# Optimization experiments

Measured on AMD Instinct MI355X. Metric: run time of the kernel, lower is better.

The kernel has to match this reference:

```python
import jax, jax.numpy as jnp
import numpy as np

D_MODEL = 1024
NUM_HEADS = 16
D_K = D_MODEL // NUM_HEADS
THETA = 10000.0
MAX_SEQ_LEN = 2048
BATCH = 2
SEQ = 2048


def setup_inputs() -> dict:
    key = jax.random.key(0)
    ks = jax.random.split(key, 5)
    std = np.sqrt(2.0 / (D_MODEL + D_MODEL)).astype(np.float32)
    x = jax.random.normal(ks[0], (BATCH, SEQ, D_MODEL), dtype=jnp.float32)
    Wq = jax.random.normal(ks[1], (D_MODEL, D_MODEL), dtype=jnp.float32) * std
    Wk = jax.random.normal(ks[2], (D_MODEL, D_MODEL), dtype=jnp.float32) * std
    Wv = jax.random.normal(ks[3], (D_MODEL, D_MODEL), dtype=jnp.float32) * std
    Wo = jax.random.normal(ks[4], (D_MODEL, D_MODEL), dtype=jnp.float32) * std
    token_positions = jnp.arange(SEQ, dtype=jnp.int32)
    return {"x": x, "token_positions": token_positions,
            "Wq": Wq, "Wk": Wk, "Wv": Wv, "Wo": Wo}


def _rope_tables(positions):
    # freqs: [d_k/2]; angles: [seq, d_k/2]
    freqs = 1.0 / (THETA ** (jnp.arange(0, D_K, 2, dtype=jnp.float32) / D_K))
    angles = positions.astype(jnp.float32)[:, None] * freqs[None, :]
    return jnp.cos(angles), jnp.sin(angles)


def _apply_rope(t, cos, sin):
    # t: [b, h, s, d_k]; cos/sin: [s, d_k/2]; interleaved pair rotation
    x1 = t[..., 0::2]
    x2 = t[..., 1::2]
    r1 = x1 * cos - x2 * sin
    r2 = x1 * sin + x2 * cos
    return jnp.stack([r1, r2], axis=-1).reshape(t.shape)


def reference(x, token_positions, Wq, Wk, Wv, Wo):
    b, s, _ = x.shape
    # projections: y = x W^T
    q = jnp.einsum('bsi,oi->bso', x, Wq)
    k = jnp.einsum('bsi,oi->bso', x, Wk)
    v = jnp.einsum('bsi,oi->bso', x, Wv)
    # split heads: [b, h, s, d]
    q = q.reshape(b, s, NUM_HEADS, D_K).transpose(0, 2, 1, 3)
    k = k.reshape(b, s, NUM_HEADS, D_K).transpose(0, 2, 1, 3)
    v = v.reshape(b, s, NUM_HEADS, D_K).transpose(0, 2, 1, 3)
    cos, sin = _rope_tables(token_positions)
    q = _apply_rope(q, cos, sin)
    k = _apply_rope(k, cos, sin)
    scale = jnp.asarray(D_K, jnp.float32) ** 0.5
    scores = jnp.einsum('bhqd,bhkd->bhqk', q, k) / scale
    causal = jnp.tril(jnp.ones((s, s), dtype=bool))
    scores = jnp.where(causal, scores, -jnp.inf)
    attn = jax.nn.softmax(scores.astype(jnp.float32), axis=-1).astype(scores.dtype)
    out = jnp.einsum('bhqk,bhkd->bhqd', attn, v)
    out = out.transpose(0, 2, 1, 3).reshape(b, s, D_MODEL)
    return jnp.einsum('bsi,oi->bso', out, Wo)
```

## Files before the change

### kernel.cpp

```cpp
#include <hip/hip_runtime.h>
#include <stdint.h>

#define D_MODEL 1024
#define NH      16
#define DKH     64
#define SEQLEN  2048
#define BATCH   2
#define KDIM    1024

typedef __attribute__((ext_vector_type(8))) short          short8;
typedef __attribute__((ext_vector_type(8))) unsigned short ushort8;
typedef __attribute__((ext_vector_type(4))) float          f32x4;

__device__ __forceinline__ unsigned short f2bf(float f) {
    union { float f; unsigned u; } v; v.f = f;
    unsigned u = v.u;
    unsigned r = (u + 0x7FFFu + ((u >> 16) & 1u)) >> 16;
    return (unsigned short)r;
}
__device__ __forceinline__ float bf2f(unsigned short h) {
    union { unsigned u; float f; } v; v.u = ((unsigned)h) << 16;
    return v.f;
}

__device__ __forceinline__ void gload_lds16(const unsigned short* g, unsigned short* l) {
    __builtin_amdgcn_global_load_lds(
        (__attribute__((address_space(1))) void*)(g),
        (__attribute__((address_space(3))) void*)(l), 16, 0, 0);
}

__global__ void cvt_all(const float* __restrict__ X,  const float* __restrict__ Wq,
                        const float* __restrict__ Wk, const float* __restrict__ Wv,
                        const float* __restrict__ Wo,
                        unsigned short* __restrict__ Xb,  unsigned short* __restrict__ Wqb,
                        unsigned short* __restrict__ Wkb, unsigned short* __restrict__ Wvb,
                        unsigned short* __restrict__ Wob) {
    const int z = blockIdx.y;
    const float* src; unsigned short* dst; int n;
    if (z == 0)      { src = X;  dst = Xb;  n = 4194304; }
    else if (z == 1) { src = Wq; dst = Wqb; n = 1048576; }
    else if (z == 2) { src = Wk; dst = Wkb; n = 1048576; }
    else if (z == 3) { src = Wv; dst = Wvb; n = 1048576; }
    else             { src = Wo; dst = Wob; n = 1048576; }
    int i = (blockIdx.x * 256 + threadIdx.x) * 8;
    if (i >= n) return;
    float4 a = *(const float4*)(src + i);
    float4 b = *(const float4*)(src + i + 4);
    ushort8 o;
    o[0] = f2bf(a.x); o[1] = f2bf(a.y); o[2] = f2bf(a.z); o[3] = f2bf(a.w);
    o[4] = f2bf(b.x); o[5] = f2bf(b.y); o[6] = f2bf(b.z); o[7] = f2bf(b.w);
    *(ushort8*)(dst + i) = o;
}

__device__ __forceinline__ void gemm_core_128(
    const unsigned short* __restrict__ A, const unsigned short* __restrict__ W,
    unsigned short* a_lds, unsigned short* b_lds,
    int m0, int n0, f32x4 acc[4][4])
{
    const int tid  = threadIdx.x;
    const int lane = tid & 63;
    const int w    = tid >> 6;
    const int quad = lane >> 4;
    const int l16  = lane & 15;
    const int wm   = w & 1, wn = w >> 1;

    const int srow = lane >> 2;
    const int scol = (lane & 3) * 8;

    #pragma unroll
    for (int mi = 0; mi < 4; mi++)
        #pragma unroll
        for (int ni = 0; ni < 4; ni++) {
            f32x4 z = {0.f, 0.f, 0.f, 0.f};
            acc[mi][ni] = z;
        }

    for (int kk = 0; kk < KDIM; kk += 32) {
        __syncthreads();
        #pragma unroll
        for (int i = 0; i < 2; ++i) {
            int c = 2 * w + i;
            gload_lds16(A + (size_t)(m0 + c * 16 + srow) * KDIM + kk + scol, &a_lds[c * 512]);
            gload_lds16(W + (size_t)(n0 + c * 16 + srow) * KDIM + kk + scol, &b_lds[c * 512]);
        }
        __syncthreads();

        short8 af[4], bf[4];
        #pragma unroll
        for (int i = 0; i < 4; i++) {
            af[i] = *(const short8*)&a_lds[(wm * 64 + i * 16 + l16) * 32 + quad * 8];
            bf[i] = *(const short8*)&b_lds[(wn * 64 + i * 16 + l16) * 32 + quad * 8];
        }
        #pragma unroll
        for (int mi = 0; mi < 4; mi++)
            #pragma unroll
            for (int ni = 0; ni < 4; ni++)
                acc[mi][ni] = __builtin_amdgcn_mfma_f32_16x16x32_bf16(af[mi], bf[ni], acc[mi][ni], 0, 0, 0);
    }
}

__global__ __launch_bounds__(256, 2)
void gemm_qkv(const unsigned short* __restrict__ X,
              const unsigned short* __restrict__ Wq,
              const unsigned short* __restrict__ Wk,
              const unsigned short* __restrict__ Wv,
              unsigned short* __restrict__ q_ws,
              unsigned short* __restrict__ k_ws,
              unsigned short* __restrict__ v_ws)
{
    __shared__ __align__(16) unsigned short a_lds[128 * 32];
    __shared__ __align__(16) unsigned short b_lds[128 * 32];

    const int z = blockIdx.z;
    const unsigned short* W = (z == 0) ? Wq : ((z == 1) ? Wk : Wv);
    const int m0 = blockIdx.x * 128, n0 = blockIdx.y * 128;

    f32x4 acc[4][4];
    gemm_core_128(X, W, a_lds, b_lds, m0, n0, acc);

    const int lane = threadIdx.x & 63;
    const int w    = threadIdx.x >> 6;
    const int quad = lane >> 4;
    const int l16  = lane & 15;
    const int wm   = w & 1, wn = w >> 1;

    #pragma unroll
    for (int mi = 0; mi < 4; mi++)
        #pragma unroll
        for (int ni = 0; ni < 4; ni++)
            #pragma unroll
            for (int r = 0; r < 4; r++) {
                int row = m0 + wm * 64 + mi * 16 + quad * 4 + r;
                int col = n0 + wn * 64 + ni * 16 + l16;
                int b = row >> 11, s = row & 2047;
                int h = col >> 6,  d = col & 63;
                int bh = b * NH + h;
                float val = acc[mi][ni][r];
                if (z == 2) {
                    v_ws[(size_t)bh * DKH * SEQLEN + (size_t)d * SEQLEN + s] = f2bf(val);
                } else {
                    unsigned short* dst = (z == 0) ? q_ws : k_ws;
                    dst[(size_t)bh * SEQLEN * DKH + (size_t)s * DKH + d] = f2bf(val);
                }
            }
}

__global__ void rope_kernel(const int* __restrict__ pos,
                            unsigned short* __restrict__ q_ws,
                            unsigned short* __restrict__ k_ws)
{
    int i = blockIdx.x * 256 + threadIdx.x;
    unsigned short* t = (i >> 19) ? k_ws : q_ws;
    int c   = i & 0x7FFFF;
    int bh  = c >> 14;
    int rem = c & 16383;
    int s   = rem >> 3;
    int ch  = rem & 7;
    size_t base = (size_t)bh * (SEQLEN * DKH) + (size_t)s * DKH + ch * 8;

    ushort8 v = *(ushort8*)(t + base);
    float p = (float)pos[s];
    ushort8 o;
    #pragma unroll
    for (int u = 0; u < 4; u++) {
        int j = ch * 4 + u;
        float freq = expf(-((float)(2 * j) * (1.0f / 64.0f)) * 9.210340371976184f);
        float ang = p * freq;
        float sn, cn;
        sincosf(ang, &sn, &cn);
        float x1 = bf2f(v[2 * u]);
        float x2 = bf2f(v[2 * u + 1]);
        o[2 * u]     = f2bf(x1 * cn - x2 * sn);
        o[2 * u + 1] = f2bf(x1 * sn + x2 * cn);
    }
    *(ushort8*)(t + base) = o;
}

__global__ __launch_bounds__(256, 2)
void attn_kernel(const unsigned short* __restrict__ q_ws,
                 const unsigned short* __restrict__ k_ws,
                 const unsigned short* __restrict__ v_ws,
                 unsigned short* __restrict__ ao)
{
    __shared__ __align__(16) unsigned short k_lds[128 * 72];
    __shared__ __align__(16) unsigned short v_lds[64 * 136];
    __shared__ __align__(16) unsigned short p_lds[4 * 16 * 136];

    const int bh  = blockIdx.x;
    const int p   = blockIdx.y;
    const int tid = threadIdx.x, lane = tid & 63, w = tid >> 6;
    const int quad = lane >> 4, l16 = lane & 15;

    const size_t kqbase = (size_t)bh * SEQLEN * DKH;
    const size_t vbase  = (size_t)bh * DKH * SEQLEN;
    const int b = bh >> 4, h = bh & 15;

    const int krow = tid >> 3, kcol = (tid & 7) * 8;
    const int vrow = tid >> 4, vcol = (tid & 15) * 8;

    #pragma unroll
    for (int phase = 0; phase < 2; ++phase) {
        const int qt  = (phase == 0) ? (31 - p) : p;
        const int q0  = qt * 64;
        const int qw0 = q0 + w * 16;
        const int nt  = (qt + 2) >> 1;

        short8 aq[2];
        #pragma unroll
        for (int kc = 0; kc < 2; kc++)
            aq[kc] = *(const short8*)(q_ws + kqbase + (size_t)(qw0 + l16) * DKH + kc * 32 + quad * 8);

        f32x4 o_acc[4];
        #pragma unroll
        for (int df = 0; df < 4; df++) { f32x4 z = {0.f,0.f,0.f,0.f}; o_acc[df] = z; }
        float l_i[4] = {0.f, 0.f, 0.f, 0.f};

        ushort8 kreg[4], vreg[4];
        #pragma unroll
        for (int rr = 0; rr < 4; ++rr) {
            kreg[rr] = *(const ushort8*)(k_ws + kqbase + (size_t)(krow + rr * 32) * DKH + kcol);
            vreg[rr] = *(const ushort8*)(v_ws + vbase + (size_t)(vrow + rr * 16) * SEQLEN + vcol);
        }

        for (int t = 0; t < nt; ++t) {
            const int s0 = t * 128;
            __syncthreads();
            #pragma unroll
            for (int rr = 0; rr < 4; ++rr) {
                *(ushort8*)&k_lds[(krow + rr * 32) * 72 + kcol]  = kreg[rr];
                *(ushort8*)&v_lds[(vrow + rr * 16) * 136 + vcol] = vreg[rr];
            }
            __syncthreads();
            if (t < nt - 1) {
                int s1 = s0 + 128;
                #pragma unroll
                for (int rr = 0; rr < 4; ++rr) {
                    kreg[rr] = *(const ushort8*)(k_ws + kqbase + (size_t)(s1 + krow + rr * 32) * DKH + kcol);
                    vreg[rr] = *(const ushort8*)(v_ws + vbase + (size_t)(vrow + rr * 16) * SEQLEN + s1 + vcol);
                }
            }

            f32x4 sf[8];
            #pragma unroll
            for (int nf = 0; nf < 8; nf++) {
                f32x4 s = {0.f,0.f,0.f,0.f};
                #pragma unroll
                for (int kc = 0; kc < 2; kc++) {
                    short8 bk = *(const short8*)&k_lds[(nf * 16 + l16) * 72 + kc * 32 + quad * 8];
                    s = __builtin_amdgcn_mfma_f32_16x16x32_bf16(aq[kc], bk, s, 0, 0, 0);
                }
                sf[nf] = s;
            }

            if (t == nt - 1) {
                #pragma unroll
                for (int nf = 0; nf < 8; nf++)
                    #pragma unroll
                    for (int r = 0; r < 4; r++) {
                        int qg = qw0 + quad * 4 + r;
                        int kg = s0 + nf * 16 + l16;
                        float pv = (kg <= qg) ? __expf(sf[nf][r] * 0.125f) : 0.f;
                        sf[nf][r] = pv;
                        l_i[r] += pv;
                    }
            } else {
                #pragma unroll
                for (int nf = 0; nf < 8; nf++)
                    #pragma unroll
                    for (int r = 0; r < 4; r++) {
                        float pv = __expf(sf[nf][r] * 0.125f);
                        sf[nf][r] = pv;
                        l_i[r] += pv;
                    }
            }

            #pragma unroll
            for (int nf = 0; nf < 8; nf++)
                #pragma unroll
                for (int r = 0; r < 4; r++)
                    p_lds[w * 2176 + (quad * 4 + r) * 136 + nf * 16 + l16] = f2bf(sf[nf][r]);

            short8 ap[4];
            #pragma unroll
            for (int kc = 0; kc < 4; kc++)
                ap[kc] = *(const short8*)&p_lds[w * 2176 + l16 * 136 + kc * 32 + quad * 8];
            #pragma unroll
            for (int df = 0; df < 4; df++)
                #pragma unroll
                for (int kc = 0; kc < 4; kc++) {
                    short8 bv = *(const short8*)&v_lds[(df * 16 + l16) * 136 + kc * 32 + quad * 8];
                    o_acc[df] = __builtin_amdgcn_mfma_f32_16x16x32_bf16(ap[kc], bv, o_acc[df], 0, 0, 0);
                }
        }

        #pragma unroll
        for (int r = 0; r < 4; r++) {
            float rs = l_i[r];
            rs += __shfl_xor(rs, 1);
            rs += __shfl_xor(rs, 2);
            rs += __shfl_xor(rs, 4);
            rs += __shfl_xor(rs, 8);
            float inv = 1.0f / rs;
            int qg = qw0 + quad * 4 + r;
            #pragma unroll
            for (int df = 0; df < 4; df++)
                ao[(size_t)(b * SEQLEN + qg) * D_MODEL + h * DKH + df * 16 + l16] =
                    f2bf(o_acc[df][r] * inv);
        }
    }
}

__global__ __launch_bounds__(256, 2)
void gemm_out(const unsigned short* __restrict__ AO,
              const unsigned short* __restrict__ Wo,
              float* __restrict__ out)
{
    __shared__ __align__(16) unsigned short a_lds[128 * 32];
    __shared__ __align__(16) unsigned short b_lds[128 * 32];

    const int m0 = blockIdx.x * 128, n0 = blockIdx.y * 128;
    f32x4 acc[4][4];
    gemm_core_128(AO, Wo, a_lds, b_lds, m0, n0, acc);

    const int lane = threadIdx.x & 63;
    const int w    = threadIdx.x >> 6;
    const int quad = lane >> 4;
    const int l16  = lane & 15;
    const int wm   = w & 1, wn = w >> 1;

    #pragma unroll
    for (int mi = 0; mi < 4; mi++)
        #pragma unroll
        for (int ni = 0; ni < 4; ni++)
            #pragma unroll
            for (int r = 0; r < 4; r++) {
                int row = m0 + wm * 64 + mi * 16 + quad * 4 + r;
                int col = n0 + wn * 64 + ni * 16 + l16;
                out[(size_t)row * D_MODEL + col] = acc[mi][ni][r];
            }
}

extern "C" void kernel_launch(void* const* d_in, const int* in_sizes, int n_in,
                              void* d_out, int out_size, void* d_ws, size_t ws_size,
                              hipStream_t stream) {
    const float* X  = (const float*)d_in[0];
    const int*   pos = (const int*)d_in[1];
    const float* Wq = (const float*)d_in[2];
    const float* Wk = (const float*)d_in[3];
    const float* Wv = (const float*)d_in[4];
    const float* Wo = (const float*)d_in[5];
    float* out = (float*)d_out;

    unsigned short* Xb  = (unsigned short*)d_ws;
    unsigned short* Wqb = Xb + 4194304;
    unsigned short* Wkb = Wqb + 1048576;
    unsigned short* Wvb = Wkb + 1048576;
    unsigned short* Wob = Wvb + 1048576;
    unsigned short* q_ws = Wob + 1048576;
    unsigned short* k_ws = q_ws + 4194304;
    unsigned short* v_ws = k_ws + 4194304;
    unsigned short* ao   = v_ws + 4194304;

    cvt_all<<<dim3(2048, 5), dim3(256), 0, stream>>>(X, Wq, Wk, Wv, Wo,
                                                     Xb, Wqb, Wkb, Wvb, Wob);
    gemm_qkv<<<dim3(32, 8, 3), dim3(256), 0, stream>>>(Xb, Wqb, Wkb, Wvb, q_ws, k_ws, v_ws);
    rope_kernel<<<dim3(4096), dim3(256), 0, stream>>>(pos, q_ws, k_ws);
    attn_kernel<<<dim3(32, 16), dim3(256), 0, stream>>>(q_ws, k_ws, v_ws, ao);
    gemm_out<<<dim3(32, 8), dim3(256), 0, stream>>>(ao, Wob, out);
}
```

Baseline: 196.2 us.

## Keep attention probabilities in registers via transposed MFMA, drop LDS round-trip

The attention kernel now computes S^T by swapping the MFMA operands, so each lane's score fragment can feed a 16x16x16 bf16 MFMA directly as the P operand. This removes the per-tile P staging through LDS and its shared-memory writes and reads. The 1/sqrt(d)·log2(e) factor is folded into Q during RoPE so exp2 replaces the scaled expf, and output stores become 4-wide vectors. Truncating bf16 packing via perm, instead of round-to-nearest, slightly changes numerics, and the PV product now uses the smaller-K MFMA instruction.

```diff
diff --git a/kernel.cpp b/kernel.cpp
--- a/kernel.cpp
+++ b/kernel.cpp
@@ -9,8 +9,12 @@
 #define KDIM    1024
 
 typedef __attribute__((ext_vector_type(8))) short          short8;
+typedef __attribute__((ext_vector_type(4))) short          bf16x4;
 typedef __attribute__((ext_vector_type(8))) unsigned short ushort8;
+typedef __attribute__((ext_vector_type(4))) unsigned short usht4;
 typedef __attribute__((ext_vector_type(4))) float          f32x4;
+
+#define QSCALE 0.18033688011112042f
 
 __device__ __forceinline__ unsigned short f2bf(float f) {
     union { float f; unsigned u; } v; v.f = f;
@@ -21,6 +25,9 @@
 __device__ __forceinline__ float bf2f(unsigned short h) {
     union { unsigned u; float f; } v; v.u = ((unsigned)h) << 16;
     return v.f;
+}
+__device__ __forceinline__ unsigned fbits(float f) {
+    union { float f; unsigned u; } v; v.f = f; return v.u;
 }
 
 __device__ __forceinline__ void gload_lds16(const unsigned short* g, unsigned short* l) {
@@ -150,7 +157,9 @@
                             unsigned short* __restrict__ k_ws)
 {
     int i = blockIdx.x * 256 + threadIdx.x;
-    unsigned short* t = (i >> 19) ? k_ws : q_ws;
+    int isK = i >> 19;
+    unsigned short* t = isK ? k_ws : q_ws;
+    float sc = isK ? 1.0f : QSCALE;
     int c   = i & 0x7FFFF;
     int bh  = c >> 14;
     int rem = c & 16383;
@@ -170,8 +179,8 @@
         sincosf(ang, &sn, &cn);
         float x1 = bf2f(v[2 * u]);
         float x2 = bf2f(v[2 * u + 1]);
-        o[2 * u]     = f2bf(x1 * cn - x2 * sn);
-        o[2 * u + 1] = f2bf(x1 * sn + x2 * cn);
+        o[2 * u]     = f2bf((x1 * cn - x2 * sn) * sc);
+        o[2 * u + 1] = f2bf((x1 * sn + x2 * cn) * sc);
     }
     *(ushort8*)(t + base) = o;
 }
@@ -184,7 +193,6 @@
 {
     __shared__ __align__(16) unsigned short k_lds[128 * 72];
     __shared__ __align__(16) unsigned short v_lds[64 * 136];
-    __shared__ __align__(16) unsigned short p_lds[4 * 16 * 136];
 
     const int bh  = blockIdx.x;
     const int p   = blockIdx.y;
@@ -213,7 +221,7 @@
         f32x4 o_acc[4];
         #pragma unroll
         for (int df = 0; df < 4; df++) { f32x4 z = {0.f,0.f,0.f,0.f}; o_acc[df] = z; }
-        float l_i[4] = {0.f, 0.f, 0.f, 0.f};
+        float lsum = 0.f;
 
         ushort8 kreg[4], vreg[4];
         #pragma unroll
@@ -240,72 +248,51 @@
                 }
             }
 
-            f32x4 sf[8];
+            const bool diag = (t == nt - 1);
             #pragma unroll
             for (int nf = 0; nf < 8; nf++) {
                 f32x4 s = {0.f,0.f,0.f,0.f};
                 #pragma unroll
                 for (int kc = 0; kc < 2; kc++) {
-                    short8 bk = *(const short8*)&k_lds[(nf * 16 + l16) * 72 + kc * 32 + quad * 8];
-                    s = __builtin_amdgcn_mfma_f32_16x16x32_bf16(aq[kc], bk, s, 0, 0, 0);
-                }
-                sf[nf] = s;
-            }
-
-            if (t == nt - 1) {
+                    short8 kf = *(const short8*)&k_lds[(nf * 16 + l16) * 72 + kc * 32 + quad * 8];
+                    s = __builtin_amdgcn_mfma_f32_16x16x32_bf16(kf, aq[kc], s, 0, 0, 0);
+                }
+                if (diag) {
+                    int qg = qw0 + l16;
+                    int kg = s0 + nf * 16 + quad * 4;
+                    #pragma unroll
+                    for (int r = 0; r < 4; r++)
+                        s[r] = (kg + r <= qg) ? __builtin_amdgcn_exp2f(s[r]) : 0.f;
+                } else {
+                    #pragma unroll
+                    for (int r = 0; r < 4; r++)
+                        s[r] = __builtin_amdgcn_exp2f(s[r]);
+                }
+                lsum += s[0] + s[1] + s[2] + s[3];
+
+                union { unsigned u[2]; bf16x4 v; } pk;
+                pk.u[0] = __builtin_amdgcn_perm(fbits(s[1]), fbits(s[0]), 0x07060302u);
+                pk.u[1] = __builtin_amdgcn_perm(fbits(s[3]), fbits(s[2]), 0x07060302u);
+
                 #pragma unroll
-                for (int nf = 0; nf < 8; nf++)
-                    #pragma unroll
-                    for (int r = 0; r < 4; r++) {
-                        int qg = qw0 + quad * 4 + r;
-                        int kg = s0 + nf * 16 + l16;
-                        float pv = (kg <= qg) ? __expf(sf[nf][r] * 0.125f) : 0.f;
-                        sf[nf][r] = pv;
-                        l_i[r] += pv;
-                    }
-            } else {
-                #pragma unroll
-                for (int nf = 0; nf < 8; nf++)
-                    #pragma unroll
-                    for (int r = 0; r < 4; r++) {
-                        float pv = __expf(sf[nf][r] * 0.125f);
-                        sf[nf][r] = pv;
-                        l_i[r] += pv;
-                    }
-            }
-
-            #pragma unroll
-            for (int nf = 0; nf < 8; nf++)
-                #pragma unroll
-                for (int r = 0; r < 4; r++)
-                    p_lds[w * 2176 + (quad * 4 + r) * 136 + nf * 16 + l16] = f2bf(sf[nf][r]);
-
-            short8 ap[4];
-            #pragma unroll
-            for (int kc = 0; kc < 4; kc++)
-                ap[kc] = *(const short8*)&p_lds[w * 2176 + l16 * 136 + kc * 32 + quad * 8];
-            #pragma unroll
-            for (int df = 0; df < 4; df++)
-                #pragma unroll
-                for (int kc = 0; kc < 4; kc++) {
-                    short8 bv = *(const short8*)&v_lds[(df * 16 + l16) * 136 + kc * 32 + quad * 8];
-                    o_acc[df] = __builtin_amdgcn_mfma_f32_16x16x32_bf16(ap[kc], bv, o_acc[df], 0, 0, 0);
-                }
-        }
-
-        #pragma unroll
-        for (int r = 0; r < 4; r++) {
-            float rs = l_i[r];
-            rs += __shfl_xor(rs, 1);
-            rs += __shfl_xor(rs, 2);
-            rs += __shfl_xor(rs, 4);
-            rs += __shfl_xor(rs, 8);
-            float inv = 1.0f / rs;
-            int qg = qw0 + quad * 4 + r;
-            #pragma unroll
-            for (int df = 0; df < 4; df++)
-                ao[(size_t)(b * SEQLEN + qg) * D_MODEL + h * DKH + df * 16 + l16] =
-                    f2bf(o_acc[df][r] * inv);
+                for (int df = 0; df < 4; df++) {
+                    bf16x4 vf = *(const bf16x4*)&v_lds[(df * 16 + l16) * 136 + nf * 16 + quad * 4];
+                    o_acc[df] = __builtin_amdgcn_mfma_f32_16x16x16bf16_1k(vf, pk.v, o_acc[df], 0, 0, 0);
+                }
+            }
+        }
+
+        float rs = lsum;
+        rs += __shfl_xor(rs, 16);
+        rs += __shfl_xor(rs, 32);
+        float inv = 1.0f / rs;
+        int qg = qw0 + l16;
+        #pragma unroll
+        for (int df = 0; df < 4; df++) {
+            usht4 ov;
+            #pragma unroll
+            for (int r = 0; r < 4; r++) ov[r] = f2bf(o_acc[df][r] * inv);
+            *(usht4*)&ao[(size_t)(b * SEQLEN + qg) * D_MODEL + h * DKH + df * 16 + quad * 4] = ov;
         }
     }
 }
```

Result: faster. 190.6 us (-2.9%).
